# Kernel optimization log

Hardware: AMD Instinct MI355X
Metric: run time of the kernel (lower is better)

The kernel has to match this reference:

```python
import jax, jax.numpy as jnp
import numpy as np

B, L, D = 4, 2048, 2048
H, KVH, HD = 16, 4, 128          # num_heads, num_kv_heads, head_dim = D // H
M = 16                           # mem_tokens
BASE = 10000.0
EPS = 1.1920929e-07              # torch F.rms_norm default eps = fp32 machine eps


def _rms_norm(x):
    # normalize over last dim, no learned weight (matches F.rms_norm(x, (hd,)))
    return x * jax.lax.rsqrt(jnp.mean(x * x, axis=-1, keepdims=True) + EPS)


def _apply_rotary(x, cos, sin):
    # x: [B, h, T, HD]; cos/sin: [1, 1, T, HD//2]
    half = x.shape[-1] // 2
    x1, x2 = x[..., :half], x[..., half:]
    return jnp.concatenate([x1 * cos + x2 * sin, -x1 * sin + x2 * cos], axis=-1)


def setup_inputs() -> dict:
    key = jax.random.key(0)
    k0, k1, k2, k3, k4 = jax.random.split(key, 5)
    kv_dim = KVH * HD
    s = 0.02
    return {
        "x": jax.random.normal(k0, (B, L, D), dtype=jnp.float32),
        "Wq": jax.random.normal(k1, (D, D), dtype=jnp.float32) * s,
        "Wk": jax.random.normal(k2, (kv_dim, D), dtype=jnp.float32) * s,
        "Wv": jax.random.normal(k3, (kv_dim, D), dtype=jnp.float32) * s,
        "Wproj": jax.random.normal(k4, (D, D), dtype=jnp.float32) * s,
        "q_gain": jnp.full((H,), 1.0, dtype=jnp.float32),
    }


def reference(x, Wq, Wk, Wv, Wproj, q_gain):
    Bx, Lx, Dx = x.shape
    # QKV projections (Linear: x @ W.T), split into heads -> [B, h, L, HD]
    q = (x @ Wq.T).reshape(Bx, Lx, H, HD).transpose(0, 2, 1, 3)
    k = (x @ Wk.T).reshape(Bx, Lx, KVH, HD).transpose(0, 2, 1, 3)
    v = (x @ Wv.T).reshape(Bx, Lx, KVH, HD).transpose(0, 2, 1, 3)
    # QK RMSNorm
    q = _rms_norm(q)
    k = _rms_norm(k)
    # RoPE on the non-memory tokens only
    T = Lx - M
    inv_freq = 1.0 / BASE ** (jnp.arange(0, HD, 2, dtype=jnp.float32) / HD)
    freqs = jnp.outer(jnp.arange(T, dtype=jnp.float32), inv_freq)  # [T, HD//2]
    cos = jnp.cos(freqs)[None, None]
    sin = jnp.sin(freqs)[None, None]
    q = jnp.concatenate([q[:, :, :M], _apply_rotary(q[:, :, M:], cos, sin)], axis=2)
    k = jnp.concatenate([k[:, :, :M], _apply_rotary(k[:, :, M:], cos, sin)], axis=2)
    # per-head gain on q
    q = q * q_gain[None, :, None, None]
    # GQA attention: group q heads by kv head (matches repeat_interleave ordering)
    rep = H // KVH
    qg = q.reshape(Bx, KVH, rep, Lx, HD)
    scale = 1.0 / np.sqrt(HD).astype(np.float32)
    scores = jnp.einsum('bgrqd,bgkd->bgrqk', qg, k) * scale  # [B, KVH, rep, L, L]
    causal = jnp.tril(jnp.ones((Lx, Lx), dtype=bool))
    scores = jnp.where(causal, scores, -jnp.inf)
    p = jax.nn.softmax(scores, axis=-1)
    y = jnp.einsum('bgrqk,bgkd->bgrqd', p, v)                # [B, KVH, rep, L, HD]
    y = y.reshape(Bx, H, Lx, HD).transpose(0, 2, 1, 3).reshape(Bx, Lx, Dx)
    return y @ Wproj.T
```

## Files before the change

### kernel.cpp

```cpp
#include <hip/hip_runtime.h>
#include <stdint.h>

typedef unsigned short u16;
typedef short s8v __attribute__((ext_vector_type(8)));
typedef float f4v __attribute__((ext_vector_type(4)));
typedef float f16v __attribute__((ext_vector_type(16)));

typedef __attribute__((address_space(1))) char gchar;
typedef __attribute__((address_space(3))) char lchar;

static __device__ __forceinline__ u16 f2bf(float f) {
  uint32_t x = __float_as_uint(f);
  x += 0x7fffu + ((x >> 16) & 1u);
  return (u16)(x >> 16);
}
static __device__ __forceinline__ float bf2f(u16 u) {
  return __uint_as_float(((uint32_t)u) << 16);
}
static __device__ __forceinline__ void gload_lds16(const void* g, void* l) {
  __builtin_amdgcn_global_load_lds((gchar*)(uintptr_t)g,
                                   (lchar*)(uint32_t)(uintptr_t)l, 16, 0, 0);
}

__global__ __launch_bounds__(256) void prep(const float4* __restrict__ x,
                                            const float4* __restrict__ wq,
                                            const float4* __restrict__ wk,
                                            const float4* __restrict__ wv,
                                            const float4* __restrict__ wp,
                                            uint2* __restrict__ xbf,
                                            uint2* __restrict__ wbf,
                                            float* __restrict__ tc,
                                            float* __restrict__ ts) {
  const int gid = blockIdx.x * 256 + threadIdx.x;
  const int st = gridDim.x * 256;
  for (int i = gid; i < 4194304; i += st) {
    float4 v = x[i];
    uint2 o;
    o.x = (uint32_t)f2bf(v.x) | ((uint32_t)f2bf(v.y) << 16);
    o.y = (uint32_t)f2bf(v.z) | ((uint32_t)f2bf(v.w) << 16);
    xbf[i] = o;
  }
  for (int i = gid; i < 2621440; i += st) {
    const float4* s;
    int off;
    if (i < 1048576)      { s = wq; off = i; }
    else if (i < 1310720) { s = wk; off = i - 1048576; }
    else if (i < 1572864) { s = wv; off = i - 1310720; }
    else                  { s = wp; off = i - 1572864; }
    float4 v = s[off];
    uint2 o;
    o.x = (uint32_t)f2bf(v.x) | ((uint32_t)f2bf(v.y) << 16);
    o.y = (uint32_t)f2bf(v.z) | ((uint32_t)f2bf(v.w) << 16);
    wbf[i] = o;
  }
  for (int i = gid; i < 2032 * 64; i += st) {
    int t = i >> 6, f = i & 63;
    float invf = 1.0f / powf(10000.0f, (float)f * (1.0f / 64.0f));
    float ang = (float)t * invf;
    float s, c;
    sincosf(ang, &s, &c);
    tc[i] = c;
    ts[i] = s;
  }
}

template <int OUT>
static __device__ __forceinline__ void gemm8_body(
    u16* sm, int bid, const u16* __restrict__ A, const u16* __restrict__ Wt,
    u16* __restrict__ Oa, float* __restrict__ OF) {
  const int tid = threadIdx.x;
  const int lane = tid & 63, wid = tid >> 6;
  const int wr = wid >> 2, wc = wid & 3;
  const int l15 = lane & 15, l4 = lane >> 4;

  const int swz = (bid & 7) * 32 + (bid >> 3);
  const int bm = swz >> 3, bn = swz & 7;
  const int m0 = bm * 256;
  const int n0r = bn * 256;

  auto pA = [&](int bs, int mh) { return sm + (bs * 2 + mh) * 8192; };
  auto pB = [&](int bs, int nh) { return sm + 32768 + (bs * 2 + nh) * 8192; };

  auto stageA = [&](int kt, int bs, int mh) {
    const int kb = kt * 64;
#pragma unroll
    for (int c = 0; c < 2; ++c) {
      int cidx = tid + c * 512;
      int rr = cidx >> 3, pc = cidx & 7;
      int grow = mh * 64 + (rr & 63) + ((rr >> 6) << 7);
      int kc = pc ^ (rr & 7);
      gload_lds16(A + (size_t)(m0 + grow) * 2048 + kb + kc * 8,
                  pA(bs, mh) + cidx * 8);
    }
  };
  auto stageB = [&](int kt, int bs, int nh) {
    const int kb = kt * 64;
#pragma unroll
    for (int c = 0; c < 2; ++c) {
      int cidx = tid + c * 512;
      int rr = cidx >> 3, pc = cidx & 7;
      int gn = ((rr >> 5) << 6) + nh * 32 + (rr & 31);
      int kc = pc ^ (rr & 7);
      gload_lds16(Wt + (size_t)(n0r + gn) * 2048 + kb + kc * 8,
                  pB(bs, nh) + cidx * 8);
    }
  };
  auto readA = [&](int bs, int mh, int i, int ks) {
    int rr = wr * 64 + i * 16 + l15;
    return *(const s8v*)&pA(bs, mh)[rr * 64 + (((ks * 4 + l4) ^ (rr & 7)) << 3)];
  };
  auto readB = [&](int bs, int nh, int j, int ks) {
    int rr = wc * 32 + j * 16 + l15;
    return *(const s8v*)&pB(bs, nh)[rr * 64 + (((ks * 4 + l4) ^ (rr & 7)) << 3)];
  };

  const f4v Z4 = {0.f, 0.f, 0.f, 0.f};
  f4v acc[8][4];
#pragma unroll
  for (int i = 0; i < 8; i++)
#pragma unroll
    for (int j = 0; j < 4; j++) acc[i][j] = Z4;

  stageA(0, 0, 0); stageA(0, 0, 1); stageB(0, 0, 0); stageB(0, 0, 1);
  stageA(1, 1, 0); stageA(1, 1, 1); stageB(1, 1, 0);
  asm volatile("s_waitcnt vmcnt(6)" ::: "memory");
  asm volatile("s_barrier" ::: "memory");

  const int NT = 32;
  for (int t = 0; t < NT; ++t) {
    const int bs = t & 1, nbs = bs ^ 1;
    s8v a[4][2], b[2][2];
#pragma unroll
    for (int i = 0; i < 4; ++i)
#pragma unroll
      for (int ks = 0; ks < 2; ++ks) a[i][ks] = readA(bs, 0, i, ks);
#pragma unroll
    for (int j = 0; j < 2; ++j)
#pragma unroll
      for (int ks = 0; ks < 2; ++ks) b[j][ks] = readB(bs, 0, j, ks);
    if (t + 1 < NT) stageB(t + 1, nbs, 1);
    asm volatile("s_barrier" ::: "memory");
    asm volatile("s_waitcnt lgkmcnt(0)" ::: "memory");
    __builtin_amdgcn_sched_barrier(0);
    __builtin_amdgcn_s_setprio(1);
#pragma unroll
    for (int i = 0; i < 4; ++i)
#pragma unroll
      for (int j = 0; j < 2; ++j)
#pragma unroll
        for (int ks = 0; ks < 2; ++ks)
          acc[i][j] = __builtin_amdgcn_mfma_f32_16x16x32_bf16(a[i][ks], b[j][ks], acc[i][j], 0, 0, 0);
    __builtin_amdgcn_s_setprio(0);
    asm volatile("s_barrier" ::: "memory");
#pragma unroll
    for (int j = 0; j < 2; ++j)
#pragma unroll
      for (int ks = 0; ks < 2; ++ks) b[j][ks] = readB(bs, 1, j, ks);
    if (t + 2 < NT) stageA(t + 2, bs, 0);
    asm volatile("s_barrier" ::: "memory");
    asm volatile("s_waitcnt lgkmcnt(0)" ::: "memory");
    __builtin_amdgcn_sched_barrier(0);
    __builtin_amdgcn_s_setprio(1);
#pragma unroll
    for (int i = 0; i < 4; ++i)
#pragma unroll
      for (int j = 0; j < 2; ++j)
#pragma unroll
        for (int ks = 0; ks < 2; ++ks)
          acc[i][2 + j] = __builtin_amdgcn_mfma_f32_16x16x32_bf16(a[i][ks], b[j][ks], acc[i][2 + j], 0, 0, 0);
    __builtin_amdgcn_s_setprio(0);
    asm volatile("s_barrier" ::: "memory");
#pragma unroll
    for (int i = 0; i < 4; ++i)
#pragma unroll
      for (int ks = 0; ks < 2; ++ks) a[i][ks] = readA(bs, 1, i, ks);
#pragma unroll
    for (int j = 0; j < 2; ++j)
#pragma unroll
      for (int ks = 0; ks < 2; ++ks) b[j][ks] = readB(bs, 0, j, ks);
    asm volatile("s_barrier" ::: "memory");
    asm volatile("s_waitcnt lgkmcnt(0)" ::: "memory");
    __builtin_amdgcn_sched_barrier(0);
    __builtin_amdgcn_s_setprio(1);
#pragma unroll
    for (int i = 0; i < 4; ++i)
#pragma unroll
      for (int j = 0; j < 2; ++j)
#pragma unroll
        for (int ks = 0; ks < 2; ++ks)
          acc[4 + i][j] = __builtin_amdgcn_mfma_f32_16x16x32_bf16(a[i][ks], b[j][ks], acc[4 + i][j], 0, 0, 0);
    __builtin_amdgcn_s_setprio(0);
    asm volatile("s_barrier" ::: "memory");
#pragma unroll
    for (int j = 0; j < 2; ++j)
#pragma unroll
      for (int ks = 0; ks < 2; ++ks) b[j][ks] = readB(bs, 1, j, ks);
    if (t + 2 < NT) { stageA(t + 2, bs, 1); stageB(t + 2, bs, 0); }
    asm volatile("s_barrier" ::: "memory");
    asm volatile("s_waitcnt lgkmcnt(0)" ::: "memory");
    __builtin_amdgcn_sched_barrier(0);
    __builtin_amdgcn_s_setprio(1);
#pragma unroll
    for (int i = 0; i < 4; ++i)
#pragma unroll
      for (int j = 0; j < 2; ++j)
#pragma unroll
        for (int ks = 0; ks < 2; ++ks)
          acc[4 + i][2 + j] = __builtin_amdgcn_mfma_f32_16x16x32_bf16(a[i][ks], b[j][ks], acc[4 + i][2 + j], 0, 0, 0);
    __builtin_amdgcn_s_setprio(0);
    if (t + 2 < NT)      asm volatile("s_waitcnt vmcnt(6)" ::: "memory");
    else if (t + 1 < NT) asm volatile("s_waitcnt vmcnt(0)" ::: "memory");
    asm volatile("s_barrier" ::: "memory");
  }

  const int colg0 = bn * 256 + wc * 64;
  if constexpr (OUT == 0) {
    const int hh = colg0 >> 7, d0 = colg0 & 127;
#pragma unroll
    for (int i = 0; i < 8; i++)
#pragma unroll
      for (int r = 0; r < 4; r++) {
        int m = m0 + wr * 128 + (i >> 2) * 64 + (i & 3) * 16 + l4 * 4 + r;
        int b2 = m >> 11, l = m & 2047;
        size_t base = ((size_t)(b2 * 16 + hh) * 2048 + l) * 128 + d0;
#pragma unroll
        for (int j = 0; j < 4; j++)
          Oa[base + (j >> 1) * 32 + (j & 1) * 16 + l15] = f2bf(acc[i][j][r]);
      }
  } else {
#pragma unroll
    for (int i = 0; i < 8; i++)
#pragma unroll
      for (int r = 0; r < 4; r++) {
        int m = m0 + wr * 128 + (i >> 2) * 64 + (i & 3) * 16 + l4 * 4 + r;
#pragma unroll
        for (int j = 0; j < 4; j++)
          OF[(size_t)m * 2048 + colg0 + (j >> 1) * 32 + (j & 1) * 16 + l15] = acc[i][j][r];
      }
  }
}

static __device__ __forceinline__ void gemm_kv_body(
    u16* sm, int bid, const u16* __restrict__ A, const u16* __restrict__ Wt,
    u16* __restrict__ Oa, u16* __restrict__ Ob2) {
  constexpr int MI = 4;
  const int tid = threadIdx.x;
  const int lane = tid & 63, wid = tid >> 6;
  const int wr = wid >> 1, wc = wid & 1;
  const int l15 = lane & 15, l4 = lane >> 4;

  const int swz = (bid & 7) * 32 + (bid >> 3);
  const int bm = swz >> 3, bn = swz & 7;
  const int m0 = bm * 256;
  const int n0r = bn * 128;

  auto pA = [&](int bs, int ks) { return sm + (bs * 2 + ks) * 8192; };
  auto pB = [&](int bs, int ks) { return sm + 32768 + (bs * 2 + ks) * 4096; };

  auto stage_part = [&](int kt, int bs, int ks) {
    const int kb = kt * 64 + ks * 32;
#pragma unroll
    for (int c = 0; c < 2; ++c) {
      int cidx = tid + c * 512;
      int r = cidx >> 2, q = cidx & 3;
      int cc = q ^ ((r >> 2) & 3);
      gload_lds16(A + (size_t)(m0 + r) * 2048 + kb + cc * 8,
                  pA(bs, ks) + cidx * 8);
    }
    {
      int cidx = tid;
      int r = cidx >> 2, q = cidx & 3;
      int cc = q ^ ((r >> 2) & 3);
      gload_lds16(Wt + (size_t)(n0r + r) * 2048 + kb + cc * 8,
                  pB(bs, ks) + cidx * 8);
    }
  };
  auto roff = [&](int fr, int c) {
    return (fr * 4 + (c ^ ((fr >> 2) & 3))) * 8;
  };

  const f4v Z4 = {0.f, 0.f, 0.f, 0.f};
  f4v acc[MI][4];
#pragma unroll
  for (int i = 0; i < MI; i++)
#pragma unroll
    for (int j = 0; j < 4; j++) acc[i][j] = Z4;

  stage_part(0, 0, 0); stage_part(0, 0, 1);
  stage_part(1, 1, 0); stage_part(1, 1, 1);

  const int NT = 32;
  for (int t = 0; t < NT; ++t) {
    const int bs = t & 1;
    if (t + 1 < NT) asm volatile("s_waitcnt vmcnt(6)" ::: "memory");
    else            asm volatile("s_waitcnt vmcnt(0)" ::: "memory");
    asm volatile("s_barrier" ::: "memory");
    const bool pf = (t + 2 < NT);
#pragma unroll
    for (int ks = 0; ks < 2; ++ks) {
      s8v afrg[MI], bfrg[4];
#pragma unroll
      for (int i = 0; i < MI; ++i)
        afrg[i] = *(const s8v*)&pA(bs, ks)[roff(wr * (MI * 16) + i * 16 + l15, l4)];
#pragma unroll
      for (int j = 0; j < 4; ++j)
        bfrg[j] = *(const s8v*)&pB(bs, ks)[roff(wc * 64 + j * 16 + l15, l4)];
      asm volatile("s_waitcnt lgkmcnt(0)" ::: "memory");
      __builtin_amdgcn_sched_barrier(0);
      asm volatile("s_barrier" ::: "memory");
      if (pf) stage_part(t + 2, bs, ks);
      __builtin_amdgcn_s_setprio(1);
#pragma unroll
      for (int i = 0; i < MI; ++i)
#pragma unroll
        for (int j = 0; j < 4; ++j)
          acc[i][j] = __builtin_amdgcn_mfma_f32_16x16x32_bf16(afrg[i], bfrg[j], acc[i][j], 0, 0, 0);
      __builtin_amdgcn_s_setprio(0);
    }
  }

  const int colg = bn * 128 + wc * 64;
  u16* Ob = (colg < 512) ? Oa : Ob2;
  const int hh = (colg & 511) >> 7, d0 = colg & 127;
#pragma unroll
  for (int i = 0; i < MI; i++)
#pragma unroll
    for (int r = 0; r < 4; r++) {
      int m = m0 + wr * (MI * 16) + i * 16 + l4 * 4 + r;
      int b = m >> 11, l = m & 2047;
      size_t base = ((size_t)(b * 4 + hh) * 2048 + l) * 128 + d0;
#pragma unroll
      for (int j = 0; j < 4; j++)
        Ob[base + j * 16 + l15] = f2bf(acc[i][j][r]);
    }
}

__global__ __launch_bounds__(512, 2) void gemm_qkv(
    const u16* __restrict__ x, const u16* __restrict__ wq,
    const u16* __restrict__ wkv, u16* __restrict__ q,
    u16* __restrict__ kO, u16* __restrict__ vO) {
  __shared__ u16 smem[65536];
  const int bid = (int)blockIdx.x;
  if (bid < 256) gemm8_body<0>(smem, bid, x, wq, q, nullptr);
  else           gemm_kv_body(smem, bid - 256, x, wkv, kO, vO);
}

__global__ __launch_bounds__(512, 2) void gemm_proj(
    const u16* __restrict__ y, const u16* __restrict__ wp, float* __restrict__ out) {
  __shared__ u16 smem[65536];
  gemm8_body<2>(smem, (int)blockIdx.x, y, wp, nullptr, out);
}

__global__ __launch_bounds__(256) void norm_transpose(
    u16* __restrict__ kbuf, const u16* __restrict__ v, u16* __restrict__ vt,
    const float* __restrict__ tc, const float* __restrict__ ts) {
  __shared__ u16 t[64][64];
  const int bid = (int)blockIdx.x;
  const int tid = threadIdx.x;
  if (bid < 1024) {
    const int l0 = (bid & 31) * 64, d0 = ((bid >> 5) & 1) * 64, bg = bid >> 6;
#pragma unroll
    for (int it = 0; it < 2; ++it) {
      int lin = it * 256 + tid;
      int r = lin >> 3, cb = lin & 7;
      s8v val = *(const s8v*)&v[((bg * 2048 + l0 + r) * 128) + d0 + cb * 8];
      *(s8v*)&t[r][(cb ^ (r & 7)) * 8] = val;
    }
    __syncthreads();
#pragma unroll
    for (int it = 0; it < 2; ++it) {
      int lin = it * 256 + tid;
      int r2 = lin >> 3, c2 = (lin & 7) * 8;
      s8v o;
#pragma unroll
      for (int j = 0; j < 8; ++j) {
        int rr = c2 + j, cc = r2;
        o[j] = (short)t[rr][(cc & 7) + 8 * ((cc >> 3) ^ (rr & 7))];
      }
      *(s8v*)&vt[((bg * 128 + d0 + r2) * 2048) + l0 + c2] = o;
    }
  } else {
    const int lane = tid & 63;
    const int gw = (bid - 1024) * 4 + (tid >> 6);
    for (int row = gw; row < 32768; row += 1024) {
      int l = row & 2047;
      u16* p = kbuf + (size_t)row * 128;
      float x1 = bf2f(p[lane]);
      float x2 = bf2f(p[lane + 64]);
      float ss = x1 * x1 + x2 * x2;
#pragma unroll
      for (int off = 32; off > 0; off >>= 1) ss += __shfl_xor(ss, off, 64);
      float r = rsqrtf(ss * (1.0f / 128.0f) + 1.1920929e-07f);
      x1 *= r; x2 *= r;
      if (l >= 16) {
        int tt = l - 16;
        float c = tc[tt * 64 + lane], s = ts[tt * 64 + lane];
        float o1 = x1 * c + x2 * s;
        float o2 = -x1 * s + x2 * c;
        x1 = o1; x2 = o2;
      }
      p[lane] = f2bf(x1);
      p[lane + 64] = f2bf(x2);
    }
  }
}

__global__ __launch_bounds__(512, 2) void attn(const u16* __restrict__ q,
                                               const u16* __restrict__ k,
                                               const u16* __restrict__ vt,
                                               u16* __restrict__ y,
                                               const float* __restrict__ qg,
                                               const float* __restrict__ tc,
                                               const float* __restrict__ ts) {
  __shared__ u16 lK[2][64 * 128];
  __shared__ u16 lVT[2][64 * 128];
  const int tid = threadIdx.x;
  const int lane = tid & 63, wid = tid >> 6;
  const int l31 = lane & 31, hi = lane >> 5;

  const int bid = (int)blockIdx.x;
  const int bg = (bid & 7) * 2 + (bid >> 7);
  const int pairi = (bid >> 3) & 15;
  const int b = bg >> 2, g = bg & 3;
  const int h = g * 4 + (wid & 3);
  const int se = wid >> 2;

  const u16* qh = q + (size_t)(b * 16 + h) * 2048 * 128;
  const u16* kb0 = k + (size_t)(b * 4 + g) * 2048 * 128;
  const u16* vtb0 = vt + (size_t)(b * 4 + g) * 128 * 2048;
  const float gscale = qg[h] * (0.08838834764831845f * 1.4426950408889634f);

  auto stage = [&](int t, int bufsel) {
    const int kv0 = t * 64;
#pragma unroll
    for (int it = 0; it < 2; ++it) {
      int lin = it * 512 + tid;
      int kj = lin >> 4, s = lin & 15;
      gload_lds16(kb0 + (size_t)(kv0 + kj) * 128 + ((s ^ (kj & 15)) * 8),
                  &lK[bufsel][lin * 8]);
    }
#pragma unroll
    for (int it = 0; it < 2; ++it) {
      int lin = it * 512 + tid;
      int r = lin >> 4, c = lin & 15;
      int gl = c ^ (r & 15);
      int d = 2 * r + (gl >> 3);
      gload_lds16(vtb0 + (size_t)d * 2048 + kv0 + ((gl & 7) * 8),
                  &lVT[bufsel][lin * 8]);
    }
  };

  for (int ph = 0; ph < 2; ++ph) {
    const int qt = ph ? (31 - pairi) : pairi;
    const int q0 = qt * 64;
    const int nt = qt + 1;
    const int pos = q0 + 32 * se + l31;

    s8v qf[8];
    {
      const u16* qp = qh + (size_t)pos * 128 + hi * 8;
      s8v qr[8];
#pragma unroll
      for (int ks = 0; ks < 8; ++ks) qr[ks] = *(const s8v*)&qp[ks * 16];
      float ssum = 0.f;
#pragma unroll
      for (int ks = 0; ks < 8; ++ks)
#pragma unroll
        for (int j = 0; j < 8; ++j) {
          float v = bf2f((u16)qr[ks][j]);
          ssum += v * v;
        }
      ssum += __shfl_xor(ssum, 32, 64);
      const float rn = rsqrtf(ssum * (1.0f / 128.0f) + 1.1920929e-07f) * gscale;
      const bool rot = (pos >= 16);
      const int tt = pos - 16;
#pragma unroll
      for (int ks = 0; ks < 4; ++ks) {
        float cv[8], sv[8];
        if (rot) {
          const float* cp = &tc[tt * 64 + ks * 16 + hi * 8];
          const float* sp = &ts[tt * 64 + ks * 16 + hi * 8];
          *(float4*)&cv[0] = *(const float4*)cp;
          *(float4*)&cv[4] = *(const float4*)(cp + 4);
          *(float4*)&sv[0] = *(const float4*)sp;
          *(float4*)&sv[4] = *(const float4*)(sp + 4);
        }
        uint32_t wlo[4], whi[4];
#pragma unroll
        for (int j2 = 0; j2 < 4; ++j2) {
          float o1[2], o2[2];
#pragma unroll
          for (int e = 0; e < 2; ++e) {
            const int j = j2 * 2 + e;
            float x1 = bf2f((u16)qr[ks][j]);
            float x2 = bf2f((u16)qr[ks + 4][j]);
            float a = x1, bb = x2;
            if (rot) { a = x1 * cv[j] + x2 * sv[j]; bb = x2 * cv[j] - x1 * sv[j]; }
            o1[e] = a * rn;
            o2[e] = bb * rn;
          }
          asm("v_cvt_pk_bf16_f32 %0, %1, %2" : "=v"(wlo[j2]) : "v"(o1[0]), "v"(o1[1]));
          asm("v_cvt_pk_bf16_f32 %0, %1, %2" : "=v"(whi[j2]) : "v"(o2[0]), "v"(o2[1]));
        }
        union { uint32_t u[4]; s8v v; } ua, ub;
        ua.u[0] = wlo[0]; ua.u[1] = wlo[1]; ua.u[2] = wlo[2]; ua.u[3] = wlo[3];
        ub.u[0] = whi[0]; ub.u[1] = whi[1]; ub.u[2] = whi[2]; ub.u[3] = whi[3];
        qf[ks] = ua.v;
        qf[ks + 4] = ub.v;
      }
    }

    f16v yacc[4];
#pragma unroll
    for (int j = 0; j < 4; ++j)
#pragma unroll
      for (int r = 0; r < 16; ++r) yacc[j][r] = 0.f;
    float mrow = -1e30f, lrow = 0.f;

    stage(0, 0);
    __syncthreads();

    for (int t = 0; t < nt; ++t) {
      const int cur = t & 1;
      if (t + 1 < nt) stage(t + 1, cur ^ 1);
      const int kv0 = t * 64;

      f16v s0a, s1a;
#pragma unroll
      for (int r = 0; r < 16; ++r) { s0a[r] = 0.f; s1a[r] = 0.f; }
      __builtin_amdgcn_s_setprio(1);
#pragma unroll
      for (int ks = 0; ks < 8; ++ks) {
        const int slot = (2 * ks + hi) ^ (l31 & 15);
        s8v kf0 = *(const s8v*)&lK[cur][(l31)*128 + slot * 8];
        s8v kf1 = *(const s8v*)&lK[cur][(32 + l31) * 128 + slot * 8];
        s0a = __builtin_amdgcn_mfma_f32_32x32x16_bf16(kf0, qf[ks], s0a, 0, 0, 0);
        s1a = __builtin_amdgcn_mfma_f32_32x32x16_bf16(kf1, qf[ks], s1a, 0, 0, 0);
      }
      __builtin_amdgcn_s_setprio(0);

      const bool last = (t == nt - 1);
      float p0[16], p1[16], mx[16];
#pragma unroll
      for (int r = 0; r < 16; ++r) {
        const int kvloc = (r & 3) + 8 * (r >> 2) + 4 * hi;
        float v0 = s0a[r];
        float v1 = s1a[r];
        if (last) {
          if (kv0 + kvloc > pos) v0 = -1e30f;
          if (kv0 + 32 + kvloc > pos) v1 = -1e30f;
        }
        p0[r] = v0; p1[r] = v1;
        mx[r] = fmaxf(v0, v1);
      }
#pragma unroll
      for (int s2 = 8; s2 > 0; s2 >>= 1)
#pragma unroll
        for (int r = 0; r < s2; ++r) mx[r] = fmaxf(mx[r], mx[r + s2]);
      float pmax = fmaxf(mx[0], __shfl_xor(mx[0], 32, 64));

      if (!__all(pmax - mrow <= 11.541560327111707f)) {
        float mnew = fmaxf(mrow, pmax);
        float corr = __builtin_amdgcn_exp2f(mrow - mnew);
#pragma unroll
        for (int r = 0; r < 16; ++r) {
          const int qloc = (r & 3) + 8 * (r >> 2) + 4 * hi;
          float cb = __shfl(corr, qloc, 64);
          yacc[0][r] *= cb; yacc[1][r] *= cb; yacc[2][r] *= cb; yacc[3][r] *= cb;
        }
        lrow *= corr;
        mrow = mnew;
      }

      float sm[16];
#pragma unroll
      for (int r = 0; r < 16; ++r) {
        float e0 = __builtin_amdgcn_exp2f(p0[r] - mrow);
        float e1 = __builtin_amdgcn_exp2f(p1[r] - mrow);
        p0[r] = e0; p1[r] = e1;
        sm[r] = e0 + e1;
      }
#pragma unroll
      for (int s2 = 8; s2 > 0; s2 >>= 1)
#pragma unroll
        for (int r = 0; r < s2; ++r) sm[r] += sm[r + s2];
      float ps = sm[0] + __shfl_xor(sm[0], 32, 64);
      lrow += ps;

      __builtin_amdgcn_s_setprio(1);
#pragma unroll
      for (int ks = 0; ks < 4; ++ks) {
        const float* pc = (ks < 2) ? p0 : p1;
        const int rb = 8 * (ks & 1);
        uint32_t A0, A1, B0, B1;
        asm("v_cvt_pk_bf16_f32 %0, %1, %2" : "=v"(A0) : "v"(pc[rb + 0]), "v"(pc[rb + 1]));
        asm("v_cvt_pk_bf16_f32 %0, %1, %2" : "=v"(A1) : "v"(pc[rb + 2]), "v"(pc[rb + 3]));
        asm("v_cvt_pk_bf16_f32 %0, %1, %2" : "=v"(B0) : "v"(pc[rb + 4]), "v"(pc[rb + 5]));
        asm("v_cvt_pk_bf16_f32 %0, %1, %2" : "=v"(B1) : "v"(pc[rb + 6]), "v"(pc[rb + 7]));
        asm("v_permlane32_swap_b32 %0, %1" : "+v"(A0), "+v"(B0));
        asm("v_permlane32_swap_b32 %0, %1" : "+v"(A1), "+v"(B1));
        union { uint32_t u[4]; s8v v; } uu;
        uu.u[0] = A0; uu.u[1] = A1; uu.u[2] = B0; uu.u[3] = B1;
#pragma unroll
        for (int jd = 0; jd < 4; ++jd) {
          const int rowd = 32 * jd + l31;
          const int line = rowd >> 1;
          const int gl = ((rowd & 1) << 3) | (2 * ks + hi);
          const int c = gl ^ (line & 15);
          s8v vf = *(const s8v*)&lVT[cur][line * 128 + c * 8];
          yacc[jd] = __builtin_amdgcn_mfma_f32_32x32x16_bf16(uu.v, vf, yacc[jd], 0, 0, 0);
        }
      }
      __builtin_amdgcn_s_setprio(0);
      __syncthreads();
    }

    float inv = 1.0f / lrow;
#pragma unroll
    for (int r = 0; r < 16; ++r) {
      const int qloc = (r & 3) + 8 * (r >> 2) + 4 * hi;
      float ib = __shfl(inv, qloc, 64);
      const int qrow = q0 + 32 * se + qloc;
      size_t base = ((size_t)(b * 2048 + qrow)) * 2048 + h * 128 + l31;
#pragma unroll
      for (int jd = 0; jd < 4; ++jd)
        y[base + 32 * jd] = f2bf(yacc[jd][r] * ib);
    }
  }
}

extern "C" void kernel_launch(void* const* d_in, const int* in_sizes, int n_in,
                              void* d_out, int out_size, void* d_ws, size_t ws_size,
                              hipStream_t stream) {
  const float* x  = (const float*)d_in[0];
  const float* Wq = (const float*)d_in[1];
  const float* Wk = (const float*)d_in[2];
  const float* Wv = (const float*)d_in[3];
  const float* Wp = (const float*)d_in[4];
  const float* qg = (const float*)d_in[5];
  float* out = (float*)d_out;

  char* ws = (char*)d_ws;
  size_t off = 0;
  auto alloc = [&](size_t bytes) {
    void* p = ws + off;
    off += (bytes + 255) & ~(size_t)255;
    return p;
  };
  u16* x_bf  = (u16*)alloc((size_t)8192 * 2048 * 2);
  u16* wq_bf = (u16*)alloc((size_t)2048 * 2048 * 2);
  u16* wk_bf = (u16*)alloc((size_t)512 * 2048 * 2);
  u16* wv_bf = (u16*)alloc((size_t)512 * 2048 * 2);
  u16* wp_bf = (u16*)alloc((size_t)2048 * 2048 * 2);
  u16* q_bf  = (u16*)alloc((size_t)4 * 16 * 2048 * 128 * 2);
  u16* k_bf  = (u16*)alloc((size_t)4 * 4 * 2048 * 128 * 2);
  u16* v_bf  = (u16*)alloc((size_t)4 * 4 * 2048 * 128 * 2);
  float* tab = (float*)alloc((size_t)2032 * 64 * 2 * 4);
  u16* y_bf  = x_bf;
  u16* vt_bf = wq_bf;
  (void)wv_bf;

  prep<<<2048, 256, 0, stream>>>((const float4*)x, (const float4*)Wq,
                                 (const float4*)Wk, (const float4*)Wv,
                                 (const float4*)Wp, (uint2*)x_bf, (uint2*)wq_bf,
                                 tab, tab + 2032 * 64);
  gemm_qkv<<<dim3(512), 512, 0, stream>>>(x_bf, wq_bf, wk_bf, q_bf, k_bf, v_bf);
  norm_transpose<<<dim3(1280), 256, 0, stream>>>(k_bf, v_bf, vt_bf,
                                                 tab, tab + 2032 * 64);
  attn<<<dim3(256), 512, 0, stream>>>(q_bf, k_bf, vt_bf, y_bf, qg,
                                      tab, tab + 2032 * 64);
  gemm_proj<<<dim3(256), 512, 0, stream>>>(y_bf, wp_bf, out);
}
```

Baseline: 325.7 us.

## Restructure GEMM main loop into K-split halves with simpler staging and swizzle

Rewrites the 256x256 bf16 GEMM main loop so that LDS holds each K-tile as two 32-wide K halves, rather than splitting it by M and N halves. Each half-step loads all 8 A and 4 B fragments per wave, then issues a full 8x4 MFMA block. The prefetch for tile t+2 is issued right after the barrier for that half. This cuts the barrier count per tile and uses a simpler 4-chunk XOR swizzle and row mapping, aiming to lower synchronisation overhead and raise MFMA density. The cost is higher register pressure from holding 12 fragments at once, and a different LDS bank-conflict pattern.

```diff
diff --git a/kernel.cpp b/kernel.cpp
--- a/kernel.cpp
+++ b/kernel.cpp
@@ -78,40 +78,30 @@
   const int m0 = bm * 256;
   const int n0r = bn * 256;
 
-  auto pA = [&](int bs, int mh) { return sm + (bs * 2 + mh) * 8192; };
-  auto pB = [&](int bs, int nh) { return sm + 32768 + (bs * 2 + nh) * 8192; };
-
-  auto stageA = [&](int kt, int bs, int mh) {
-    const int kb = kt * 64;
+  auto pA = [&](int bs, int ks) { return sm + (bs * 2 + ks) * 8192; };
+  auto pB = [&](int bs, int ks) { return sm + 32768 + (bs * 2 + ks) * 8192; };
+
+  auto stage_part = [&](int kt, int bs, int ks) {
+    const int kb = kt * 64 + ks * 32;
 #pragma unroll
     for (int c = 0; c < 2; ++c) {
       int cidx = tid + c * 512;
-      int rr = cidx >> 3, pc = cidx & 7;
-      int grow = mh * 64 + (rr & 63) + ((rr >> 6) << 7);
-      int kc = pc ^ (rr & 7);
-      gload_lds16(A + (size_t)(m0 + grow) * 2048 + kb + kc * 8,
-                  pA(bs, mh) + cidx * 8);
-    }
-  };
-  auto stageB = [&](int kt, int bs, int nh) {
-    const int kb = kt * 64;
+      int r = cidx >> 2, q = cidx & 3;
+      int cc = q ^ ((r >> 2) & 3);
+      gload_lds16(A + (size_t)(m0 + r) * 2048 + kb + cc * 8,
+                  pA(bs, ks) + cidx * 8);
+    }
 #pragma unroll
     for (int c = 0; c < 2; ++c) {
       int cidx = tid + c * 512;
-      int rr = cidx >> 3, pc = cidx & 7;
-      int gn = ((rr >> 5) << 6) + nh * 32 + (rr & 31);
-      int kc = pc ^ (rr & 7);
-      gload_lds16(Wt + (size_t)(n0r + gn) * 2048 + kb + kc * 8,
-                  pB(bs, nh) + cidx * 8);
+      int r = cidx >> 2, q = cidx & 3;
+      int cc = q ^ ((r >> 2) & 3);
+      gload_lds16(Wt + (size_t)(n0r + r) * 2048 + kb + cc * 8,
+                  pB(bs, ks) + cidx * 8);
     }
   };
-  auto readA = [&](int bs, int mh, int i, int ks) {
-    int rr = wr * 64 + i * 16 + l15;
-    return *(const s8v*)&pA(bs, mh)[rr * 64 + (((ks * 4 + l4) ^ (rr & 7)) << 3)];
-  };
-  auto readB = [&](int bs, int nh, int j, int ks) {
-    int rr = wc * 32 + j * 16 + l15;
-    return *(const s8v*)&pB(bs, nh)[rr * 64 + (((ks * 4 + l4) ^ (rr & 7)) << 3)];
+  auto roff = [&](int fr, int c) {
+    return (fr * 4 + (c ^ ((fr >> 2) & 3))) * 8;
   };
 
   const f4v Z4 = {0.f, 0.f, 0.f, 0.f};
@@ -121,121 +111,62 @@
 #pragma unroll
     for (int j = 0; j < 4; j++) acc[i][j] = Z4;
 
-  stageA(0, 0, 0); stageA(0, 0, 1); stageB(0, 0, 0); stageB(0, 0, 1);
-  stageA(1, 1, 0); stageA(1, 1, 1); stageB(1, 1, 0);
-  asm volatile("s_waitcnt vmcnt(6)" ::: "memory");
-  asm volatile("s_barrier" ::: "memory");
+  stage_part(0, 0, 0); stage_part(0, 0, 1);
+  stage_part(1, 1, 0); stage_part(1, 1, 1);
 
   const int NT = 32;
   for (int t = 0; t < NT; ++t) {
-    const int bs = t & 1, nbs = bs ^ 1;
-    s8v a[4][2], b[2][2];
-#pragma unroll
-    for (int i = 0; i < 4; ++i)
-#pragma unroll
-      for (int ks = 0; ks < 2; ++ks) a[i][ks] = readA(bs, 0, i, ks);
-#pragma unroll
-    for (int j = 0; j < 2; ++j)
-#pragma unroll
-      for (int ks = 0; ks < 2; ++ks) b[j][ks] = readB(bs, 0, j, ks);
-    if (t + 1 < NT) stageB(t + 1, nbs, 1);
+    const int bs = t & 1;
+    if (t + 1 < NT) asm volatile("s_waitcnt vmcnt(8)" ::: "memory");
+    else            asm volatile("s_waitcnt vmcnt(0)" ::: "memory");
     asm volatile("s_barrier" ::: "memory");
-    asm volatile("s_waitcnt lgkmcnt(0)" ::: "memory");
-    __builtin_amdgcn_sched_barrier(0);
-    __builtin_amdgcn_s_setprio(1);
-#pragma unroll
-    for (int i = 0; i < 4; ++i)
-#pragma unroll
-      for (int j = 0; j < 2; ++j)
-#pragma unroll
-        for (int ks = 0; ks < 2; ++ks)
-          acc[i][j] = __builtin_amdgcn_mfma_f32_16x16x32_bf16(a[i][ks], b[j][ks], acc[i][j], 0, 0, 0);
-    __builtin_amdgcn_s_setprio(0);
-    asm volatile("s_barrier" ::: "memory");
-#pragma unroll
-    for (int j = 0; j < 2; ++j)
-#pragma unroll
-      for (int ks = 0; ks < 2; ++ks) b[j][ks] = readB(bs, 1, j, ks);
-    if (t + 2 < NT) stageA(t + 2, bs, 0);
-    asm volatile("s_barrier" ::: "memory");
-    asm volatile("s_waitcnt lgkmcnt(0)" ::: "memory");
-    __builtin_amdgcn_sched_barrier(0);
-    __builtin_amdgcn_s_setprio(1);
-#pragma unroll
-    for (int i = 0; i < 4; ++i)
-#pragma unroll
-      for (int j = 0; j < 2; ++j)
-#pragma unroll
-        for (int ks = 0; ks < 2; ++ks)
-          acc[i][2 + j] = __builtin_amdgcn_mfma_f32_16x16x32_bf16(a[i][ks], b[j][ks], acc[i][2 + j], 0, 0, 0);
-    __builtin_amdgcn_s_setprio(0);
-    asm volatile("s_barrier" ::: "memory");
-#pragma unroll
-    for (int i = 0; i < 4; ++i)
-#pragma unroll
-      for (int ks = 0; ks < 2; ++ks) a[i][ks] = readA(bs, 1, i, ks);
-#pragma unroll
-    for (int j = 0; j < 2; ++j)
-#pragma unroll
-      for (int ks = 0; ks < 2; ++ks) b[j][ks] = readB(bs, 0, j, ks);
-    asm volatile("s_barrier" ::: "memory");
-    asm volatile("s_waitcnt lgkmcnt(0)" ::: "memory");
-    __builtin_amdgcn_sched_barrier(0);
-    __builtin_amdgcn_s_setprio(1);
-#pragma unroll
-    for (int i = 0; i < 4; ++i)
-#pragma unroll
-      for (int j = 0; j < 2; ++j)
-#pragma unroll
-        for (int ks = 0; ks < 2; ++ks)
-          acc[4 + i][j] = __builtin_amdgcn_mfma_f32_16x16x32_bf16(a[i][ks], b[j][ks], acc[4 + i][j], 0, 0, 0);
-    __builtin_amdgcn_s_setprio(0);
-    asm volatile("s_barrier" ::: "memory");
-#pragma unroll
-    for (int j = 0; j < 2; ++j)
-#pragma unroll
-      for (int ks = 0; ks < 2; ++ks) b[j][ks] = readB(bs, 1, j, ks);
-    if (t + 2 < NT) { stageA(t + 2, bs, 1); stageB(t + 2, bs, 0); }
-    asm volatile("s_barrier" ::: "memory");
-    asm volatile("s_waitcnt lgkmcnt(0)" ::: "memory");
-    __builtin_amdgcn_sched_barrier(0);
-    __builtin_amdgcn_s_setprio(1);
-#pragma unroll
-    for (int i = 0; i < 4; ++i)
-#pragma unroll
-      for (int j = 0; j < 2; ++j)
-#pragma unroll
-        for (int ks = 0; ks < 2; ++ks)
-          acc[4 + i][2 + j] = __builtin_amdgcn_mfma_f32_16x16x32_bf16(a[i][ks], b[j][ks], acc[4 + i][2 + j], 0, 0, 0);
-    __builtin_amdgcn_s_setprio(0);
-    if (t + 2 < NT)      asm volatile("s_waitcnt vmcnt(6)" ::: "memory");
-    else if (t + 1 < NT) asm volatile("s_waitcnt vmcnt(0)" ::: "memory");
-    asm volatile("s_barrier" ::: "memory");
-  }
-
-  const int colg0 = bn * 256 + wc * 64;
+    const bool pf = (t + 2 < NT);
+#pragma unroll
+    for (int ks = 0; ks < 2; ++ks) {
+      s8v a[8], b[4];
+#pragma unroll
+      for (int i = 0; i < 8; ++i)
+        a[i] = *(const s8v*)&pA(bs, ks)[roff(wr * 128 + i * 16 + l15, l4)];
+#pragma unroll
+      for (int j = 0; j < 4; ++j)
+        b[j] = *(const s8v*)&pB(bs, ks)[roff(wc * 64 + j * 16 + l15, l4)];
+      asm volatile("s_waitcnt lgkmcnt(0)" ::: "memory");
+      __builtin_amdgcn_sched_barrier(0);
+      asm volatile("s_barrier" ::: "memory");
+      if (pf) stage_part(t + 2, bs, ks);
+      __builtin_amdgcn_s_setprio(1);
+#pragma unroll
+      for (int i = 0; i < 8; ++i)
+#pragma unroll
+        for (int j = 0; j < 4; ++j)
+          acc[i][j] = __builtin_amdgcn_mfma_f32_16x16x32_bf16(a[i], b[j], acc[i][j], 0, 0, 0);
+      __builtin_amdgcn_s_setprio(0);
+    }
+  }
+
+  const int colg = bn * 256 + wc * 64;
   if constexpr (OUT == 0) {
-    const int hh = colg0 >> 7, d0 = colg0 & 127;
+    const int hh = colg >> 7, d0 = colg & 127;
 #pragma unroll
     for (int i = 0; i < 8; i++)
 #pragma unroll
       for (int r = 0; r < 4; r++) {
-        int m = m0 + wr * 128 + (i >> 2) * 64 + (i & 3) * 16 + l4 * 4 + r;
+        int m = m0 + wr * 128 + i * 16 + l4 * 4 + r;
         int b2 = m >> 11, l = m & 2047;
         size_t base = ((size_t)(b2 * 16 + hh) * 2048 + l) * 128 + d0;
 #pragma unroll
         for (int j = 0; j < 4; j++)
-          Oa[base + (j >> 1) * 32 + (j & 1) * 16 + l15] = f2bf(acc[i][j][r]);
+          Oa[base + j * 16 + l15] = f2bf(acc[i][j][r]);
       }
   } else {
 #pragma unroll
     for (int i = 0; i < 8; i++)
 #pragma unroll
       for (int r = 0; r < 4; r++) {
-        int m = m0 + wr * 128 + (i >> 2) * 64 + (i & 3) * 16 + l4 * 4 + r;
+        int m = m0 + wr * 128 + i * 16 + l4 * 4 + r;
 #pragma unroll
         for (int j = 0; j < 4; j++)
-          OF[(size_t)m * 2048 + colg0 + (j >> 1) * 32 + (j & 1) * 16 + l15] = acc[i][j][r];
+          OF[(size_t)m * 2048 + colg + j * 16 + l15] = acc[i][j][r];
       }
   }
 }
```

New measurement: 324.8 us (median of 2 runs). Within noise of the previous version (-0.3%).
